# Performance work log

Measured on AMD Instinct MI355X. Metric: run time of the kernel, lower is better.

Reference implementation:

```python
import jax, jax.numpy as jnp
import numpy as np

N_SITES, NODE_F = 50000, 64
N_PERM, N_NEIGH = 12, 8
IN_F = N_NEIGH * NODE_F  # 512
OUT_F = 64
LN2 = float(np.log(2.0))


def setup_inputs() -> dict:
    key = jax.random.key(0)
    k1, k2, k3, k4 = jax.random.split(key, 4)
    X_sites = jax.random.normal(k1, (N_SITES, NODE_F), dtype=jnp.float32)
    X_NSs = jax.random.randint(k2, (N_SITES, N_PERM, N_NEIGH), 0, N_SITES)
    # nn.Linear(IN_F, OUT_F): weight (OUT_F, IN_F), bias (OUT_F,)
    bound = 1.0 / np.sqrt(IN_F)
    W = jax.random.uniform(k3, (OUT_F, IN_F), minval=-bound, maxval=bound, dtype=jnp.float32)
    b = jax.random.uniform(k4, (OUT_F,), minval=-bound, maxval=bound, dtype=jnp.float32)
    return {"X_sites": X_sites, "X_NSs": X_NSs, "W": W, "b": b}


def reference(X_sites, X_NSs, W, b):
    # Gather neighbor features: (N, P, K, F) -> (N, P, K*F)
    gathered = X_sites[X_NSs].reshape(X_NSs.shape[0], N_PERM, IN_F)
    # Linear: (N, P, IN_F) @ (IN_F, OUT_F) + b
    x1 = jnp.einsum('npi,oi->npo', gathered, W) + b
    # Shifted softplus: softplus(x) - log(2)  (dropout treated as identity / eval mode)
    x2 = jax.nn.softplus(x1) - LN2
    # Sum over permutations -> (N, OUT_F)
    return x2.sum(axis=1)
```

## Files before the change

### kernel.cpp

```cpp
#include <hip/hip_runtime.h>
#include <hip/hip_bf16.h>

#define N_SITES 50000
#define N_PERM  12
#define N_NEIGH 8
#define NODE_F  64
#define IN_F    512
#define OUT_F   64
#define N_TILES (N_SITES / 16)
#define LN2F    0.69314718055994530942f

#define XCHUNKS (N_SITES * NODE_F / 8)
#define WCHUNKS (OUT_F * IN_F / 8)
#define SLOT_E  520
#define BUF_E   (16 * SLOT_E)

typedef __bf16 bf16x8 __attribute__((ext_vector_type(8)));
typedef float  f32x4  __attribute__((ext_vector_type(4)));

__device__ __forceinline__ unsigned short f32_to_bf16_rne(unsigned int u) {
    u += 0x7FFFu + ((u >> 16) & 1u);
    return (unsigned short)(u >> 16);
}

__device__ __forceinline__ int probe_is_bf16(const void* Xorig) {
    int lane = threadIdx.x & 63;
    unsigned short h = ((const unsigned short*)Xorig)[2 * lane];
    int e = (h >> 7) & 0xFF;
    unsigned long long mm = __ballot(e >= 110 && e <= 140);
    return (__popcll(mm) >= 48) ? 1 : 0;
}

__device__ __forceinline__ void pack8(const uint4* src, uint4* dst, int c) {
    uint4 a = src[2 * c], b = src[2 * c + 1];
    uint4 o;
    o.x = (unsigned int)f32_to_bf16_rne(a.x) | ((unsigned int)f32_to_bf16_rne(a.y) << 16);
    o.y = (unsigned int)f32_to_bf16_rne(a.z) | ((unsigned int)f32_to_bf16_rne(a.w) << 16);
    o.z = (unsigned int)f32_to_bf16_rne(b.x) | ((unsigned int)f32_to_bf16_rne(b.y) << 16);
    o.w = (unsigned int)f32_to_bf16_rne(b.z) | ((unsigned int)f32_to_bf16_rne(b.w) << 16);
    dst[c] = o;
}

__global__ void convert_all(const void* __restrict__ Xv, const void* __restrict__ Wv,
                            const void* __restrict__ Bv, uint4* __restrict__ Xb,
                            uint4* __restrict__ Wb, float* __restrict__ Bf) {
    const int isbf = probe_is_bf16(Xv);
    int c = blockIdx.x * blockDim.x + threadIdx.x;
    if (c < XCHUNKS) {
        if (isbf) Xb[c] = ((const uint4*)Xv)[c];
        else      pack8((const uint4*)Xv, Xb, c);
    } else if (c < XCHUNKS + WCHUNKS) {
        int cw = c - XCHUNKS;
        if (isbf) Wb[cw] = ((const uint4*)Wv)[cw];
        else      pack8((const uint4*)Wv, Wb, cw);
    } else if (c < XCHUNKS + WCHUNKS + OUT_F) {
        int i = c - XCHUNKS - WCHUNKS;
        Bf[i] = isbf ? (float)((const __bf16*)Bv)[i] : ((const float*)Bv)[i];
    }
}

__device__ __forceinline__ float softplus_sh(float x) {
    float t = __expf(-fabsf(x));
    return fmaxf(x, 0.f) + 0.69314718056f * __log2f(1.f + t);
}

__device__ __forceinline__ void async16(const __bf16* g, __bf16* l) {
    __builtin_amdgcn_global_load_lds(
        (const __attribute__((address_space(1))) unsigned int*)g,
        (__attribute__((address_space(3))) unsigned int*)l, 16, 0, 0);
}


#define BARX(N) do {                                                          \
        asm volatile("s_waitcnt vmcnt(" #N ") lgkmcnt(0)" ::: "memory");      \
        __builtin_amdgcn_s_barrier();                                         \
        asm volatile("" ::: "memory");                                        \
    } while (0)

__global__ __launch_bounds__(256, 3)
void lcnn_dma(const void* __restrict__ Xorig, const __bf16* __restrict__ Xb,
              const int* __restrict__ NS, const __bf16* __restrict__ Wb,
              const float* __restrict__ Bf, void* __restrict__ outv)
{
    __shared__ __align__(16) __bf16 Abuf[3][BUF_E];

    const int wave = threadIdx.x >> 6;
    const int lane = threadIdx.x & 63;
    const int m    = lane & 15;
    const int quad = lane >> 4;
    const int mk   = m & 7;
    const int mh   = m >> 3;
    const int tile = blockIdx.x;

    bf16x8 Wfrag[16];
    #pragma unroll
    for (int ks = 0; ks < 16; ++ks)
        Wfrag[ks] = *(const bf16x8*)(Wb + (size_t)(wave * 16 + m) * IN_F + ks * 32 + quad * 8);

    const float bias = Bf[wave * 16 + m];

    const int srow = lane >> 3;
    const int csrc = (lane & 7) ^ srow;
    const int* ns0 = NS + (size_t)(tile * 16 + srow)     * (N_PERM * N_NEIGH) + wave * 2;
    const int* ns1 = NS + (size_t)(tile * 16 + srow + 8) * (N_PERM * N_NEIGH) + wave * 2;

    int4 idx[N_PERM];
    #pragma unroll
    for (int p = 0; p < N_PERM; ++p) {
        idx[p].x = ns0[p * N_NEIGH];     idx[p].y = ns1[p * N_NEIGH];
        idx[p].z = ns0[p * N_NEIGH + 1]; idx[p].w = ns1[p * N_NEIGH + 1];
    }

    auto stagep = [&](int bslot, int4 iv) {
        async16(Xb + (size_t)iv.x * NODE_F + csrc * 8, &Abuf[bslot][(wave * 4 + 0) * SLOT_E]);
        async16(Xb + (size_t)iv.y * NODE_F + csrc * 8, &Abuf[bslot][(wave * 4 + 1) * SLOT_E]);
        async16(Xb + (size_t)iv.z * NODE_F + csrc * 8, &Abuf[bslot][(wave * 4 + 2) * SLOT_E]);
        async16(Xb + (size_t)iv.w * NODE_F + csrc * 8, &Abuf[bslot][(wave * 4 + 3) * SLOT_E]);
    };

    stagep(0, idx[0]);
    stagep(1, idx[1]);
    BARX(4);

    f32x4 sum = {0.f, 0.f, 0.f, 0.f};
    #pragma unroll
    for (int p = 0; p < N_PERM; ++p) {
        if (p < N_PERM - 2) stagep((p + 2) % 3, idx[p + 2]);

        f32x4 acc = {0.f, 0.f, 0.f, 0.f};
        const __bf16* bb = &Abuf[p % 3][0];
        #pragma unroll
        for (int ks = 0; ks < 16; ++ks) {
            int t_r = (ks >> 1) * 2 + mh;
            int j   = ((ks & 1) << 2) | quad;
            bf16x8 afr = *(const bf16x8*)(bb + t_r * SLOT_E + mk * 64 + ((j ^ mk) << 3));
            acc = __builtin_amdgcn_mfma_f32_16x16x32_bf16(afr, Wfrag[ks], acc, 0, 0, 0);
        }
        #pragma unroll
        for (int r = 0; r < 4; ++r) sum[r] += softplus_sh(acc[r] + bias);

        if (p < N_PERM - 2)      BARX(4);
        else if (p < N_PERM - 1) BARX(0);
    }

    const int isbf = probe_is_bf16(Xorig);
    #pragma unroll
    for (int r = 0; r < 4; ++r) {
        size_t pos = (size_t)(tile * 16 + quad * 4 + r) * OUT_F + wave * 16 + m;
        float v = sum[r] - 12.0f * LN2F;
        if (isbf) ((__bf16*)outv)[pos] = (__bf16)v;
        else      ((float*)outv)[pos]  = v;
    }
}

__global__ void lcnn_fallback(const float* __restrict__ X, const int* __restrict__ NS,
                              const float* __restrict__ W, const float* __restrict__ B,
                              float* __restrict__ out) {
    int t = blockIdx.x * blockDim.x + threadIdx.x;
    if (t >= N_SITES * OUT_F) return;
    int sitei = t >> 6, o = t & 63;
    const int* ns = NS + (size_t)sitei * 96;
    float s = 0.f;
    for (int p = 0; p < N_PERM; ++p) {
        float x = B[o];
        for (int n = 0; n < N_NEIGH; ++n) {
            const float* xr = X + (size_t)ns[p * 8 + n] * NODE_F;
            const float* wr = W + (size_t)o * IN_F + n * NODE_F;
            for (int f = 0; f < NODE_F; ++f) x += xr[f] * wr[f];
        }
        s += softplus_sh(x);
    }
    out[t] = s - 12.0f * LN2F;
}

extern "C" void kernel_launch(void* const* d_in, const int* in_sizes, int n_in,
                              void* d_out, int out_size, void* d_ws, size_t ws_size,
                              hipStream_t stream) {
    const void* X  = d_in[0];
    const int*  NS = (const int*)d_in[1];
    const void* W  = d_in[2];
    const void* B  = d_in[3];

    char* ws = (char*)d_ws;
    __bf16* Xb = (__bf16*)ws;
    __bf16* Wb = (__bf16*)(ws + (size_t)XCHUNKS * 16);
    float*  Bf = (float*)(ws + (size_t)(XCHUNKS + WCHUNKS) * 16);
    const bool conv = ws_size >= (size_t)(XCHUNKS + WCHUNKS) * 16 + OUT_F * 4;

    if (conv) {
        int nch = XCHUNKS + WCHUNKS + OUT_F;
        hipLaunchKernelGGL(convert_all, dim3((nch + 255) / 256), dim3(256), 0, stream,
                           X, W, B, (uint4*)Xb, (uint4*)Wb, Bf);
        hipLaunchKernelGGL(lcnn_dma, dim3(N_TILES), dim3(256), 0, stream,
                           X, Xb, NS, Wb, Bf, d_out);
    } else {
        hipLaunchKernelGGL(lcnn_fallback,
                           dim3((N_SITES * OUT_F + 255) / 256), dim3(256), 0, stream,
                           (const float*)X, NS, (const float*)W, (const float*)B,
                           (float*)d_out);
    }
}
```

Before: 141.9 us.

## Split K across wave pairs with LDS partial-sum exchange and deferred softplus

Each wave now computes two 16-column output fragments over half the K dimension instead of one fragment over all of K, so each A fragment loaded from LDS feeds two MFMAs. Waves with kh=1 write their partial accumulators to a double-buffered LDS exchange area, and kh=0 waves add them in during the next permutation before applying softplus, which overlaps the epilogue with the next MMA phase. The change aims to halve A-fragment LDS reads per MFMA, but it adds LDS traffic for the partials, leaves half the waves idle in the epilogue, and lowers the launch-bounds occupancy hint from 3 to 2 blocks.

```diff
diff --git a/kernel.cpp b/kernel.cpp
--- a/kernel.cpp
+++ b/kernel.cpp
@@ -77,27 +77,34 @@
         asm volatile("" ::: "memory");                                        \
     } while (0)
 
-__global__ __launch_bounds__(256, 3)
+__global__ __launch_bounds__(256, 2)
 void lcnn_dma(const void* __restrict__ Xorig, const __bf16* __restrict__ Xb,
               const int* __restrict__ NS, const __bf16* __restrict__ Wb,
               const float* __restrict__ Bf, void* __restrict__ outv)
 {
     __shared__ __align__(16) __bf16 Abuf[3][BUF_E];
+    __shared__ __align__(16) float  Xch[2][2][8][64];
 
     const int wave = threadIdx.x >> 6;
     const int lane = threadIdx.x & 63;
+    const int fh   = wave & 1;
+    const int kh   = wave >> 1;
     const int m    = lane & 15;
     const int quad = lane >> 4;
     const int mk   = m & 7;
     const int mh   = m >> 3;
     const int tile = blockIdx.x;
 
-    bf16x8 Wfrag[16];
+    bf16x8 Wfrag[8][2];
     #pragma unroll
-    for (int ks = 0; ks < 16; ++ks)
-        Wfrag[ks] = *(const bf16x8*)(Wb + (size_t)(wave * 16 + m) * IN_F + ks * 32 + quad * 8);
-
-    const float bias = Bf[wave * 16 + m];
+    for (int ksl = 0; ksl < 8; ++ksl) {
+        #pragma unroll
+        for (int nf = 0; nf < 2; ++nf)
+            Wfrag[ksl][nf] = *(const bf16x8*)(Wb + (size_t)(fh * 32 + nf * 16 + m) * IN_F
+                                              + (kh * 8 + ksl) * 32 + quad * 8);
+    }
+    const float bias0 = Bf[fh * 32 + m];
+    const float bias1 = Bf[fh * 32 + 16 + m];
 
     const int srow = lane >> 3;
     const int csrc = (lane & 7) ^ srow;
@@ -122,34 +129,74 @@
     stagep(1, idx[1]);
     BARX(4);
 
-    f32x4 sum = {0.f, 0.f, 0.f, 0.f};
+    f32x4 sum0 = {0.f, 0.f, 0.f, 0.f}, sum1 = {0.f, 0.f, 0.f, 0.f};
+    f32x4 accP0 = {0.f, 0.f, 0.f, 0.f}, accP1 = {0.f, 0.f, 0.f, 0.f};
+
     #pragma unroll
     for (int p = 0; p < N_PERM; ++p) {
         if (p < N_PERM - 2) stagep((p + 2) % 3, idx[p + 2]);
 
-        f32x4 acc = {0.f, 0.f, 0.f, 0.f};
+        if (p > 0 && kh == 0) {
+            #pragma unroll
+            for (int r = 0; r < 4; ++r) {
+                sum0[r] += softplus_sh(accP0[r] + Xch[(p - 1) & 1][fh][r][lane]     + bias0);
+                sum1[r] += softplus_sh(accP1[r] + Xch[(p - 1) & 1][fh][r + 4][lane] + bias1);
+            }
+        }
+
+        f32x4 acc0 = {0.f, 0.f, 0.f, 0.f};
+        f32x4 acc1 = {0.f, 0.f, 0.f, 0.f};
         const __bf16* bb = &Abuf[p % 3][0];
         #pragma unroll
-        for (int ks = 0; ks < 16; ++ks) {
+        for (int ksl = 0; ksl < 8; ++ksl) {
+            int ks  = kh * 8 + ksl;
             int t_r = (ks >> 1) * 2 + mh;
             int j   = ((ks & 1) << 2) | quad;
             bf16x8 afr = *(const bf16x8*)(bb + t_r * SLOT_E + mk * 64 + ((j ^ mk) << 3));
-            acc = __builtin_amdgcn_mfma_f32_16x16x32_bf16(afr, Wfrag[ks], acc, 0, 0, 0);
-        }
-        #pragma unroll
-        for (int r = 0; r < 4; ++r) sum[r] += softplus_sh(acc[r] + bias);
+            acc0 = __builtin_amdgcn_mfma_f32_16x16x32_bf16(afr, Wfrag[ksl][0], acc0, 0, 0, 0);
+            acc1 = __builtin_amdgcn_mfma_f32_16x16x32_bf16(afr, Wfrag[ksl][1], acc1, 0, 0, 0);
+        }
+
+        if (kh) {
+            #pragma unroll
+            for (int r = 0; r < 4; ++r) {
+                Xch[p & 1][fh][r][lane]     = acc0[r];
+                Xch[p & 1][fh][r + 4][lane] = acc1[r];
+            }
+        } else {
+            accP0 = acc0;
+            accP1 = acc1;
+        }
 
         if (p < N_PERM - 2)      BARX(4);
         else if (p < N_PERM - 1) BARX(0);
-    }
-
-    const int isbf = probe_is_bf16(Xorig);
-    #pragma unroll
-    for (int r = 0; r < 4; ++r) {
-        size_t pos = (size_t)(tile * 16 + quad * 4 + r) * OUT_F + wave * 16 + m;
-        float v = sum[r] - 12.0f * LN2F;
-        if (isbf) ((__bf16*)outv)[pos] = (__bf16)v;
-        else      ((float*)outv)[pos]  = v;
+        else {
+            asm volatile("s_waitcnt lgkmcnt(0)" ::: "memory");
+            __builtin_amdgcn_s_barrier();
+            asm volatile("" ::: "memory");
+        }
+    }
+
+    if (kh == 0) {
+        #pragma unroll
+        for (int r = 0; r < 4; ++r) {
+            sum0[r] += softplus_sh(accP0[r] + Xch[1][fh][r][lane]     + bias0);
+            sum1[r] += softplus_sh(accP1[r] + Xch[1][fh][r + 4][lane] + bias1);
+        }
+        const int isbf = probe_is_bf16(Xorig);
+        #pragma unroll
+        for (int r = 0; r < 4; ++r) {
+            size_t pos = (size_t)(tile * 16 + quad * 4 + r) * OUT_F + fh * 32 + m;
+            float v0 = sum0[r] - 12.0f * LN2F;
+            float v1 = sum1[r] - 12.0f * LN2F;
+            if (isbf) {
+                ((__bf16*)outv)[pos]      = (__bf16)v0;
+                ((__bf16*)outv)[pos + 16] = (__bf16)v1;
+            } else {
+                ((float*)outv)[pos]      = v0;
+                ((float*)outv)[pos + 16] = v1;
+            }
+        }
     }
 }
 
```

Result: slower. 173.0 us (+21.9%).
